# Optimization experiments

Measured on AMD Instinct MI355X. Metric: run time of the kernel, lower is better.

Reference implementation:

```python
import jax, jax.numpy as jnp
import numpy as np

B, S, D, H, F, REF = 4, 1024, 512, 8, 2048, 2
HGRID = 32   # sqrt(seq_len)
HALF = 3     # 7x7 window -> half-width 3


def _masks():
    i = jnp.arange(HGRID)
    near = jnp.abs(i[:, None] - i[None, :]) <= HALF            # [h,h]
    inside = (near[:, None, :, None] & near[None, :, None, :]).reshape(S, S)
    # reverse=True mask (mca): outside-window -> -inf, inside -> 0
    m_rev = jnp.where(inside, 0.0, -jnp.inf).astype(jnp.float32)
    # reverse=False mask (msa/nsa): inside-window -> -inf, outside -> 0 (faithful to source)
    m_fwd = jnp.where(inside, -jnp.inf, 0.0).astype(jnp.float32)
    return m_rev, m_fwd


def _mha(q, k, v, w, b, ow, ob, mask):
    # torch nn.MultiheadAttention, batch_first, eval mode (no dropout)
    hd = D // H
    wq, wk, wv = jnp.split(w, 3, axis=0)
    bq, bk, bv = jnp.split(b, 3)

    def proj(t, wt, bt):
        Bt, Lt = t.shape[0], t.shape[1]
        return (t @ wt.T + bt).reshape(Bt, Lt, H, hd).transpose(0, 2, 1, 3)

    qh, kh, vh = proj(q, wq, bq), proj(k, wk, bk), proj(v, wv, bv)
    scores = jnp.einsum('bhqd,bhkd->bhqk', qh, kh) / jnp.sqrt(jnp.float32(hd))
    if mask is not None:
        scores = scores + mask
    a = jax.nn.softmax(scores, axis=-1)
    o = jnp.einsum('bhqk,bhkd->bhqd', a, vh).transpose(0, 2, 1, 3).reshape(q.shape[0], q.shape[1], D)
    return o @ ow.T + ob


def _ln(x, g, b, eps=1e-5):
    m = x.mean(-1, keepdims=True)
    v = ((x - m) ** 2).mean(-1, keepdims=True)
    return (x - m) / jnp.sqrt(v + eps) * g + b


def setup_inputs() -> dict:
    key = jax.random.key(0)
    ks = jax.random.split(key, 16)
    d = {}
    d['x'] = jax.random.normal(ks[0], (B, S, D), jnp.float32)
    d['ref_mca'] = jax.random.normal(ks[1], (B, REF * S, D), jnp.float32)
    d['gate'] = jax.random.uniform(ks[2], (B, S, 5), jnp.float32)
    i = 3
    for p in ['mca', 'ca', 'msa', 'nsa', 'sa']:
        d[p + '_w'] = 0.02 * jax.random.normal(ks[i], (3 * D, D), jnp.float32); i += 1
        d[p + '_b'] = jnp.zeros((3 * D,), jnp.float32)
        d[p + '_ow'] = 0.02 * jax.random.normal(ks[i], (D, D), jnp.float32); i += 1
        d[p + '_ob'] = jnp.zeros((D,), jnp.float32)
    d['ln1_g'] = jnp.ones((D,), jnp.float32); d['ln1_b'] = jnp.zeros((D,), jnp.float32)
    d['ln2_g'] = jnp.ones((D,), jnp.float32); d['ln2_b'] = jnp.zeros((D,), jnp.float32)
    d['fc1_w'] = 0.02 * jax.random.normal(ks[i], (F, D), jnp.float32); i += 1
    d['fc1_b'] = jnp.zeros((F,), jnp.float32)
    d['fc2_w'] = 0.02 * jax.random.normal(ks[i], (D, F), jnp.float32); i += 1
    d['fc2_b'] = jnp.zeros((D,), jnp.float32)
    return d


def reference(x, ref_mca, gate,
              mca_w, mca_b, mca_ow, mca_ob,
              ca_w, ca_b, ca_ow, ca_ob,
              msa_w, msa_b, msa_ow, msa_ob,
              nsa_w, nsa_b, nsa_ow, nsa_ob,
              sa_w, sa_b, sa_ow, sa_ob,
              ln1_g, ln1_b, ln2_g, ln2_b,
              fc1_w, fc1_b, fc2_w, fc2_b):
    m_rev, m_fwd = _masks()
    # mca branch: sum attention over each seq_len chunk of ref_mca (window-inside mask)
    mca_x = jnp.zeros_like(x)
    for r in range(REF):
        chunk = ref_mca[:, r * S:(r + 1) * S, :]
        mca_x = mca_x + _mha(x, chunk, chunk, mca_w, mca_b, mca_ow, mca_ob, m_rev)
    # faithful to source: loop variable leaks, so ca/nsa use the LAST chunk
    ref_last = ref_mca[:, (REF - 1) * S:, :]
    new_x = gate[:, :, 0:1] * mca_x
    new_x = new_x + gate[:, :, 1:2] * _mha(x, ref_last, ref_last, ca_w, ca_b, ca_ow, ca_ob, None)
    new_x = new_x + gate[:, :, 2:3] * _mha(x, x, x, msa_w, msa_b, msa_ow, msa_ob, m_fwd)
    new_x = new_x + gate[:, :, 3:4] * _mha(x, ref_last, x, nsa_w, nsa_b, nsa_ow, nsa_ob, m_fwd)
    new_x = new_x + gate[:, :, 4:5] * _mha(x, x, x, sa_w, sa_b, sa_ow, sa_ob, None)
    h = _ln(new_x, ln1_g, ln1_b)
    y = jax.nn.gelu(h @ fc1_w.T + fc1_b, approximate=False) @ fc2_w.T + fc2_b
    return _ln(h + y, ln2_g, ln2_b)
```

## Files before the change

### kernel.cpp

```cpp
#include <hip/hip_runtime.h>

typedef __bf16 bf16_t;
typedef bf16_t bf16x8 __attribute__((ext_vector_type(8)));
typedef float f32x4v __attribute__((ext_vector_type(4)));
typedef unsigned int u32;
typedef unsigned long long u64;

__device__ __forceinline__ void gload16(const bf16_t* g, bf16_t* l) {
    __builtin_amdgcn_global_load_lds((const __attribute__((address_space(1))) u32*)g,
                                     (__attribute__((address_space(3))) u32*)l, 16, 0, 0);
}

#define QSCALE 0.18033688011112042f

struct PackBDesc {
    int nseg;
    int blkOf[21];
    const float* src[20];
    bf16_t* dst[20];
    int chunks[20];
    int dstLd[20];
    int shift[20];
};

__global__ __launch_bounds__(256) void packb_k(PackBDesc d) {
    int b = blockIdx.x;
    int s = 0;
    while (s + 1 < d.nseg && b >= d.blkOf[s + 1]) ++s;
    int idx = (b - d.blkOf[s]) * 256 + threadIdx.x;
    if (idx >= d.chunks[s]) return;
    const float* src = d.src[s] + (size_t)idx * 8;
    int r = idx >> d.shift[s];
    int c8 = idx & ((1 << d.shift[s]) - 1);
    bf16_t* dst = d.dst[s] + (size_t)r * d.dstLd[s] + (size_t)c8 * 8;
    float4 v0 = reinterpret_cast<const float4*>(src)[0];
    float4 v1 = reinterpret_cast<const float4*>(src)[1];
    bf16x8 o;
    o[0] = (bf16_t)v0.x; o[1] = (bf16_t)v0.y; o[2] = (bf16_t)v0.z; o[3] = (bf16_t)v0.w;
    o[4] = (bf16_t)v1.x; o[5] = (bf16_t)v1.y; o[6] = (bf16_t)v1.z; o[7] = (bf16_t)v1.w;
    *reinterpret_cast<bf16x8*>(dst) = o;
}

struct PackFDesc {
// ... 109 lines not shown

struct ProjDesc {
    const bf16_t* A[3];
    int aBS[3], aRowOff[3];
    const bf16_t* B[3];
    const float* bias[3];
    bf16_t* Out[3];
    int ldo[3];
    int ntn[3], base[3];
    u64 qmask[3];
};

__global__ __launch_bounds__(256) void proj_k(ProjDesc d) {
    int wg = (blockIdx.x & 7) * 272 + (blockIdx.x >> 3);
    int s = (wg >= d.base[2]) ? 2 : (wg >= d.base[1]) ? 1 : 0;
    int local = wg - d.base[s];
    int tn = local % d.ntn[s];
    int tm = local / d.ntn[s];
    gemm_core<0, 128, 128>(tm, tn, 0, d.A[s], d.aBS[s], d.aRowOff[s], 512,
                           d.B[s], d.bias[s], d.Out[s], d.ldo[s], 0, nullptr, nullptr, 0, 512,
                           d.qmask[s]);
}

template <int EPI, int BM, int BN>
__global__ __launch_bounds__(256) void gemmT(
    const bf16_t* __restrict__ A, int aBS, int aRowOff, int lda,
    const bf16_t* __restrict__ B, const float* __restrict__ bias,
    void* __restrict__ Out, int ldo, size_t outSplitStride,
    const float* __restrict__ gate, const float* __restrict__ obcat, int kPerSplit) {
    gemm_core<EPI, BM, BN>(blockIdx.y, blockIdx.x, blockIdx.z, A, aBS, aRowOff, lda, B, bias,
                           Out, ldo, outSplitStride, gate, obcat, blockIdx.z * kPerSplit, kPerSplit, 0);
}

struct AttnDesc {
    const bf16_t* Q[6];
    const bf16_t* K[6];
    const bf16_t* V[6];
    int ldq[6], ldk[6], ldv[6];
    int segOff[6], gidx[6], mask[6];
    bf16_t* acat;
    const float* gate;
};

__global__ __launch_bounds__(512) void attn7_k(AttnDesc d) {
    __shared__ __attribute__((aligned(16))) bf16_t Ks[2][64][72];
    __shared__ __attribute__((aligned(16))) bf16_t Vt[2][64][72];
    __shared__ __attribute__((aligned(16))) bf16_t Ps[8][16][40];

    const int bid = blockIdx.x;
    const int u = bid % 6;
    const int rem = bid / 6;
    const int qt = rem & 3;
    const int lg = rem >> 2;
    const int h = lg & 7, b = lg >> 3;
    const int mask = d.mask[u];

    const int tid = threadIdx.x;
    const int lane = tid & 63;
    const int w = tid >> 6;
    const int l15 = lane & 15, l16 = lane >> 4;

    const int qbase = qt * 256 + w * 32;
    const int qrow = b * 1024 + qbase;
    const int qblk = qbase >> 5;
    const int ldq = d.ldq[u], ldk = d.ldk[u], ldv = d.ldv[u];

    bf16x8 aq[2][2];
#pragma unroll
    for (int t = 0; t < 2; ++t)
#pragma unroll
        for (int s = 0; s < 2; ++s)
            aq[t][s] = *reinterpret_cast<const bf16x8*>(
                d.Q[u] + (size_t)(qrow + t * 16 + l15) * ldq + h * 64 + s * 32 + l16 * 8);

    float mrow0 = -1e30f, mrow1 = -1e30f, lsum0 = 0.f, lsum1 = 0.f;
    f32x4v accO[2][4] = {};

    const int srow = tid >> 3, scol8 = (tid & 7) * 8;
    const int vcol = srow ^ ((tid & 7) << 3);
    const bf16_t* kbase = d.K[u] + (size_t)(b * 1024) * ldk + h * 64 + scol8;
    const bf16_t* vbase = d.V[u] + (size_t)(b * 1024) * ldv + h * 64 + scol8;

    int t0, t1;
    if (mask == 1) {
        int klo = qt * 8 - 3;  if (klo < 0) klo = 0;
        int khi = qt * 8 + 10; if (khi > 31) khi = 31;
        t0 = klo >> 1; t1 = (khi >> 1) + 1;
    } else { t0 = 0; t1 = 16; }

    auto ldKV = [&](int tt, bf16x8& k, bf16x8& v) {
        k = *reinterpret_cast<const bf16x8*>(kbase + (size_t)(tt * 64 + srow) * ldk);
        v = *reinterpret_cast<const bf16x8*>(vbase + (size_t)(tt * 64 + srow) * ldv);
    };
    auto stKV = [&](int buf, const bf16x8& k, const bf16x8& v) {
        *reinterpret_cast<bf16x8*>(&Ks[buf][srow][scol8]) = k;
#pragma unroll
        for (int j = 0; j < 8; ++j) Vt[buf][scol8 + j][vcol] = v[j];
    };

    bf16x8 rk, rv, rk2, rv2;
    ldKV(t0, rk, rv);
    stKV(0, rk, rv);
    __syncthreads();

    int cur = 0;
    for (int tt = t0; tt < t1; ++tt) {
        if (tt + 1 < t1) ldKV(tt + 1, rk2, rv2);

        int bd0 = qblk - tt * 2;     if (bd0 < 0) bd0 = -bd0;
        int bd1 = qblk - tt * 2 - 1; if (bd1 < 0) bd1 = -bd1;
        const bool a0 = (mask != 1) || (bd0 <= 3);
        const bool a1 = (mask != 1) || (bd1 <= 3);
        if (a0 || a1) {
            f32x4v z[2][4];
#pragma unroll
            for (int nt = 0; nt < 4; ++nt) {
                bf16x8 kf0 = *reinterpret_cast<const bf16x8*>(&Ks[cur][nt * 16 + l15][l16 * 8]);
                bf16x8 kf1 = *reinterpret_cast<const bf16x8*>(&Ks[cur][nt * 16 + l15][32 + l16 * 8]);
                f32x4v z0 = {}, z1 = {};
                z0 = __builtin_amdgcn_mfma_f32_16x16x32_bf16(kf0, aq[0][0], z0, 0, 0, 0);
                z0 = __builtin_amdgcn_mfma_f32_16x16x32_bf16(kf1, aq[0][1], z0, 0, 0, 0);
                z1 = __builtin_amdgcn_mfma_f32_16x16x32_bf16(kf0, aq[1][0], z1, 0, 0, 0);
                z1 = __builtin_amdgcn_mfma_f32_16x16x32_bf16(kf1, aq[1][1], z1, 0, 0, 0);
                z[0][nt] = z0; z[1][nt] = z1;
            }
            float p[2][4][4];
#pragma unroll
            for (int t = 0; t < 2; ++t) {
                const int qgt = t * 16 + l15;
#pragma unroll
                for (int nt = 0; nt < 4; ++nt) {
                    const int bd = (nt >> 1) ? bd1 : bd0;
                    const bool act = (nt >> 1) ? a1 : a0;
                    const bool needMask = (mask == 1) || (mask == 2 && bd <= 3);
#pragma unroll
                    for (int i = 0; i < 4; ++i) {
                        float v = z[t][nt][i];
                        if (!act) v = -1e30f;
                        else if (needMask) {
                            int k5 = (nt & 1) * 16 + l16 * 4 + i;
                            int dq = qgt - k5; if (dq < 0) dq = -dq;
                            bool inside = (bd <= 3) && (dq <= 3);
                            if (mask == 1 ? !inside : inside) v = -1e30f;
                        }
                        p[t][nt][i] = v;
                    }
                }
            }
            float tmx0 = p[0][0][0], tmx1 = p[1][0][0];
#pragma unroll
            for (int nt = 0; nt < 4; ++nt)
#pragma unroll
                for (int i = 0; i < 4; ++i) {
                    tmx0 = fmaxf(tmx0, p[0][nt][i]);
                    tmx1 = fmaxf(tmx1, p[1][nt][i]);
                }
            tmx0 = fmaxf(tmx0, __shfl_xor(tmx0, 16, 64));
            tmx0 = fmaxf(tmx0, __shfl_xor(tmx0, 32, 64));
            tmx1 = fmaxf(tmx1, __shfl_xor(tmx1, 16, 64));
            tmx1 = fmaxf(tmx1, __shfl_xor(tmx1, 32, 64));
            float grow = fmaxf(tmx0 - mrow0, tmx1 - mrow1);
            if (!__all(grow <= 8.0f)) {
                float mn0 = fmaxf(mrow0, tmx0), mn1 = fmaxf(mrow1, tmx1);
                float f0 = exp2f(mrow0 - mn0), f1 = exp2f(mrow1 - mn1);
                mrow0 = mn0; mrow1 = mn1;
                lsum0 *= f0; lsum1 *= f1;
                float fq0[4], fq1[4];
#pragma unroll
                for (int i = 0; i < 4; ++i) {
                    fq0[i] = __shfl(f0, l16 * 4 + i, 64);
                    fq1[i] = __shfl(f1, l16 * 4 + i, 64);
                }
#pragma unroll
                for (int dblk = 0; dblk < 4; ++dblk)
#pragma unroll
                    for (int i = 0; i < 4; ++i) {
                        accO[0][dblk][i] *= fq0[i];
                        accO[1][dblk][i] *= fq1[i];
                    }
            }
            float rs0 = 0.f, rs1 = 0.f;
#pragma unroll
            for (int nt = 0; nt < 4; ++nt)
#pragma unroll
                for (int i = 0; i < 4; ++i) {
                    p[0][nt][i] = exp2f(p[0][nt][i] - mrow0); rs0 += p[0][nt][i];
                    p[1][nt][i] = exp2f(p[1][nt][i] - mrow1); rs1 += p[1][nt][i];
                }
            rs0 += __shfl_xor(rs0, 16, 64); rs0 += __shfl_xor(rs0, 32, 64);
            rs1 += __shfl_xor(rs1, 16, 64); rs1 += __shfl_xor(rs1, 32, 64);
            lsum0 += rs0; lsum1 += rs1;

#pragma unroll
            for (int kh = 0; kh < 2; ++kh) {
#pragma unroll
                for (int n = 0; n < 2; ++n)
#pragma unroll
                    for (int i = 0; i < 4; ++i)
                        Ps[w][l15][n * 16 + l16 * 4 + i] = (bf16_t)p[0][kh * 2 + n][i];
                bf16x8 pa0 = *reinterpret_cast<const bf16x8*>(&Ps[w][l15][l16 * 8]);
#pragma unroll
                for (int n = 0; n < 2; ++n)
#pragma unroll
                    for (int i = 0; i < 4; ++i)
                        Ps[w][l15][n * 16 + l16 * 4 + i] = (bf16_t)p[1][kh * 2 + n][i];
                bf16x8 pa1 = *reinterpret_cast<const bf16x8*>(&Ps[w][l15][l16 * 8]);
#pragma unroll
                for (int dblk = 0; dblk < 4; ++dblk) {
                    int dd = dblk * 16 + l15;
                    int csw = ((kh * 4 + l16) ^ (dd >> 3)) * 8;
                    bf16x8 bv = *reinterpret_cast<const bf16x8*>(&Vt[cur][dd][csw]);
                    accO[0][dblk] = __builtin_amdgcn_mfma_f32_16x16x32_bf16(pa0, bv, accO[0][dblk], 0, 0, 0);
                    accO[1][dblk] = __builtin_amdgcn_mfma_f32_16x16x32_bf16(pa1, bv, accO[1][dblk], 0, 0, 0);
                }
            }
        }

        if (tt + 1 < t1) stKV(cur ^ 1, rk2, rv2);
        __syncthreads();
        cur ^= 1;
    }

    float inv0 = 1.0f / lsum0, inv1 = 1.0f / lsum1;
    float iq0[4], iq1[4];
#pragma unroll
    for (int i = 0; i < 4; ++i) {
        iq0[i] = __shfl(inv0, l16 * 4 + i, 64);
        iq1[i] = __shfl(inv1, l16 * 4 + i, 64);
    }
#pragma unroll
    for (int dblk = 0; dblk < 4; ++dblk)
#pragma unroll
        for (int i = 0; i < 4; ++i) {
            int r0 = qrow + l16 * 4 + i;
            int r1 = r0 + 16;
            float g0 = d.gate[(size_t)r0 * 5 + d.gidx[u]];
            float g1 = d.gate[(size_t)r1 * 5 + d.gidx[u]];
            d.acat[(size_t)r0 * 3072 + d.segOff[u] + h * 64 + dblk * 16 + l15] =
                (bf16_t)(accO[0][dblk][i] * iq0[i] * g0);
            d.acat[(size_t)r1 * 3072 + d.segOff[u] + h * 64 + dblk * 16 + l15] =
                (bf16_t)(accO[1][dblk][i] * iq1[i] * g1);
        }
}

__global__ __launch_bounds__(256) void ln_k(const float* __restrict__ in0,
                                            const float* __restrict__ in1,
                                            const float* __restrict__ in2,
                                            const float* __restrict__ g,
                                            const float* __restrict__ bb,
                                            float* __restrict__ outf,
                                            bf16_t* __restrict__ outb) {
    __shared__ float red[8];
    int row = blockIdx.x;
    int t = threadIdx.x;
    float x0 = in0[(size_t)row * 512 + t];
    float x1 = in0[(size_t)row * 512 + 256 + t];
    if (in1) {
        x0 += in1[(size_t)row * 512 + t];
        x1 += in1[(size_t)row * 512 + 256 + t];
    }
    if (in2) {
        x0 += in2[(size_t)row * 512 + t];
        x1 += in2[(size_t)row * 512 + 256 + t];
    }
    float s = x0 + x1, sq = x0 * x0 + x1 * x1;
#pragma unroll
    for (int d = 1; d < 64; d <<= 1) {
        s += __shfl_xor(s, d, 64);
        sq += __shfl_xor(sq, d, 64);
    }
    int w = t >> 6;
    if ((t & 63) == 0) { red[w] = s; red[4 + w] = sq; }
    __syncthreads();
    s = red[0] + red[1] + red[2] + red[3];
    sq = red[4] + red[5] + red[6] + red[7];
// ... 26 lines not shown
        ow[p] = (const float*)d_in[5 + p * 4];
        ob[p] = (const float*)d_in[6 + p * 4];
    }
    const float* ln1_g = (const float*)d_in[23];
    const float* ln1_b = (const float*)d_in[24];
    const float* ln2_g = (const float*)d_in[25];
    const float* ln2_b = (const float*)d_in[26];
    const float* fc1_w = (const float*)d_in[27];
    const float* fc1_b = (const float*)d_in[28];
    const float* fc2_w = (const float*)d_in[29];
    const float* fc2_b = (const float*)d_in[30];

    char* ws = (char*)d_ws;
    size_t off = 0;
    auto alloc = [&](size_t bytes) {
        char* p = ws + off;
        off += (bytes + 255) & ~(size_t)255;
        return p;
    };
    const size_t S2 = (size_t)4096 * 512;
    bf16_t* xb    = (bf16_t*)alloc(S2 * 2);
    bf16_t* refb  = (bf16_t*)alloc((size_t)8192 * 512 * 2);
    bf16_t* Wxp   = (bf16_t*)alloc((size_t)5120 * 512 * 2);
    bf16_t* WRp   = (bf16_t*)alloc((size_t)2560 * 512 * 2);
    bf16_t* Wop   = (bf16_t*)alloc((size_t)512 * 3072 * 2);
    bf16_t* fc1p  = (bf16_t*)alloc((size_t)2048 * 512 * 2);
    bf16_t* fc2p  = (bf16_t*)alloc((size_t)512 * 2048 * 2);
    float*  bxp   = (float*)alloc((size_t)5120 * 4);
    float*  brp   = (float*)alloc((size_t)2560 * 4);
    float*  obc   = (float*)alloc((size_t)5 * 512 * 4);
    bf16_t* XP    = (bf16_t*)alloc((size_t)4096 * 5120 * 2);
    bf16_t* RP    = (bf16_t*)alloc((size_t)4096 * 2560 * 2);
    bf16_t* R0    = (bf16_t*)alloc((size_t)4096 * 1024 * 2);
    bf16_t* acat  = (bf16_t*)alloc((size_t)4096 * 3072 * 2);
    float*  newx  = (float*)alloc(S2 * 4 * 2);
    float*  hbuf  = (float*)alloc(S2 * 4);
    bf16_t* hb  = refb;
    bf16_t* ub  = XP;
    float*  yp  = newx;

    PackBDesc pb{};
    int nb = 0, blk = 0;
    auto addB = [&](const float* s, bf16_t* dptr, int chunks, int dstLd, int shift) {
        pb.src[nb] = s; pb.dst[nb] = dptr; pb.chunks[nb] = chunks;
        pb.dstLd[nb] = dstLd; pb.shift[nb] = shift;
        pb.blkOf[nb] = blk; blk += (chunks + 255) / 256; ++nb;
    };
    auto addLin = [&](const float* s, bf16_t* dptr, long elems) {
        addB(s, dptr, (int)(elems / 8), 0, 30);
    };
    addLin(x, xb, (long)4096 * 512);
    addLin(ref_mca, refb, (long)8192 * 512);
    addLin(w[0], Wxp, (long)512 * 512);
    addLin(w[1], Wxp + (size_t)512 * 512, (long)512 * 512);
    addLin(w[2], Wxp + (size_t)1024 * 512, (long)1536 * 512);
    addLin(w[3], Wxp + (size_t)2560 * 512, (long)512 * 512);
    addLin(w[3] + (size_t)1024 * 512, Wxp + (size_t)3072 * 512, (long)512 * 512);
    addLin(w[4], Wxp + (size_t)3584 * 512, (long)1536 * 512);
    addLin(w[0] + (size_t)512 * 512, WRp, (long)1024 * 512);
    addLin(w[1] + (size_t)512 * 512, WRp + (size_t)1024 * 512, (long)1024 * 512);
    addLin(w[3] + (size_t)512 * 512, WRp + (size_t)2048 * 512, (long)512 * 512);
    const float* owSeg[6] = {ow[0], ow[0], ow[1], ow[2], ow[3], ow[4]};
    for (int s = 0; s < 6; ++s)
        addB(owSeg[s], Wop + (size_t)s * 512, 32768, 3072, 6);
    addLin(fc1_w, fc1p, (long)2048 * 512);
    addLin(fc2_w, fc2p, (long)512 * 2048);
    pb.nseg = nb; pb.blkOf[nb] = blk;
    packb_k<<<blk, 256, 0, stream>>>(pb);

    PackFDesc pf{};
    int nf = 0, fblk = 0;
    auto addF = [&](const float* s, float* dptr, int n) {
        pf.src[nf] = s; pf.dst[nf] = dptr; pf.n[nf] = n;
        pf.blkOf[nf] = fblk; fblk += (n + 255) / 256; ++nf;
    };
    addF(wb[0], bxp, 512);
    addF(wb[1], bxp + 512, 512);
    addF(wb[2], bxp + 1024, 1536);
    addF(wb[3], bxp + 2560, 512);
    addF(wb[3] + 1024, bxp + 3072, 512);
    addF(wb[4], bxp + 3584, 1536);
    addF(wb[0] + 512, brp, 1024);
    addF(wb[1] + 512, brp + 1024, 1024);
    addF(wb[3] + 512, brp + 2048, 512);
    for (int p = 0; p < 5; ++p) addF(ob[p], obc + p * 512, 512);
    pf.nseg = nf; pf.blkOf[nf] = fblk;
    packf_k<<<fblk, 256, 0, stream>>>(pf);

    ProjDesc pd{};
    pd.A[0] = xb;   pd.aBS[0] = 1024; pd.aRowOff[0] = 0;    pd.B[0] = Wxp; pd.bias[0] = bxp; pd.Out[0] = XP; pd.ldo[0] = 5120; pd.ntn[0] = 40;
    pd.A[1] = refb; pd.aBS[1] = 2048; pd.aRowOff[1] = 1024; pd.B[1] = WRp; pd.bias[1] = brp; pd.Out[1] = RP; pd.ldo[1] = 2560; pd.ntn[1] = 20;
    pd.A[2] = refb; pd.aBS[2] = 2048; pd.aRowOff[2] = 0;    pd.B[2] = WRp; pd.bias[2] = brp; pd.Out[2] = R0; pd.ldo[2] = 1024; pd.ntn[2] = 8;
    pd.base[0] = 0; pd.base[1] = 40 * 32; pd.base[2] = 40 * 32 + 20 * 32;
    pd.qmask[0] = 0xF0F00FFFULL; pd.qmask[1] = 0; pd.qmask[2] = 0;
    proj_k<<<(40 + 20 + 8) * 32, 256, 0, stream>>>(pd);

    AttnDesc ad{};
    auto setU = [&](int u, const bf16_t* Q, int lq, const bf16_t* K, int lk,
                    const bf16_t* V, int lv, int seg, int gi, int mk) {
        ad.Q[u] = Q; ad.ldq[u] = lq; ad.K[u] = K; ad.ldk[u] = lk; ad.V[u] = V; ad.ldv[u] = lv;
        ad.segOff[u] = seg; ad.gidx[u] = gi; ad.mask[u] = mk;
    };
    setU(0, XP, 5120, R0, 1024, R0 + 512, 1024, 0, 0, 1);
    setU(1, XP, 5120, RP, 2560, RP + 512, 2560, 512, 0, 1);
    setU(2, XP + 512, 5120, RP + 1024, 2560, RP + 1536, 2560, 1024, 1, 0);
    setU(3, XP + 1024, 5120, XP + 1536, 5120, XP + 2048, 5120, 1536, 2, 2);
    setU(4, XP + 2560, 5120, RP + 2048, 2560, XP + 3072, 5120, 2048, 3, 2);
    setU(5, XP + 3584, 5120, XP + 4096, 5120, XP + 4608, 5120, 2560, 4, 0);
    ad.acat = acat; ad.gate = gate;
    attn7_k<<<768, 512, 0, stream>>>(ad);

    gemmT<4, 64, 64><<<dim3(8, 64, 2), 256, 0, stream>>>(acat, 1024, 0, 3072, Wop, nullptr,
                                                         newx, 512, S2, gate, obc, 1536);
    ln_k<<<4096, 256, 0, stream>>>(newx, newx + S2, nullptr, ln1_g, ln1_b, hbuf, hb);
    gemmT<1, 128, 128><<<dim3(16, 32, 1), 256, 0, stream>>>(hb, 1024, 0, 512, fc1p, fc1_b,
                                                            ub, 2048, 0, nullptr, nullptr, 512);
    gemmT<3, 64, 64><<<dim3(8, 64, 2), 256, 0, stream>>>(ub, 1024, 0, 2048, fc2p, fc2_b,
                                                         yp, 512, S2, nullptr, nullptr, 1024);
    ln_k<<<4096, 256, 0, stream>>>(hbuf, yp, yp + S2, ln2_g, ln2_b, (float*)d_out, nullptr);
}
```

Before: 351.2 us.

## Pre-transpose V into global buffer and read K/V directly in attention

```diff
diff --git a/kernel.cpp b/kernel.cpp
--- a/kernel.cpp
+++ b/kernel.cpp
@@ -184,26 +184,53 @@
                            Out, ldo, outSplitStride, gate, obcat, blockIdx.z * kPerSplit, kPerSplit, 0);
 }
 
+struct VTDesc {
+    const bf16_t* V[6];
+    int ldv[6];
+    bf16_t* VT;
+};
+
+__global__ __launch_bounds__(256) void vtrans_k(VTDesc d) {
+    __shared__ __attribute__((aligned(16))) bf16_t T[64][72];
+    int bid = blockIdx.x;
+    int kt = bid & 15;
+    int h = (bid >> 4) & 7;
+    int b = (bid >> 7) & 3;
+    int u = bid >> 9;
+    const int ldv = d.ldv[u];
+    const bf16_t* src = d.V[u] + (size_t)(b * 1024 + kt * 64) * ldv + h * 64;
+    int t = threadIdx.x;
+    int r = t >> 2, c0 = (t & 3) * 16;
+    *reinterpret_cast<bf16x8*>(&T[r][c0]) =
+        *reinterpret_cast<const bf16x8*>(src + (size_t)r * ldv + c0);
+    *reinterpret_cast<bf16x8*>(&T[r][c0 + 8]) =
+        *reinterpret_cast<const bf16x8*>(src + (size_t)r * ldv + c0 + 8);
+    __syncthreads();
+    bf16_t* dst = d.VT + (((size_t)u * 4 + b) * 8 + h) * 65536 + (size_t)r * 1024 + kt * 64 + c0;
+    bf16x8 o1, o2;
+#pragma unroll
+    for (int j = 0; j < 8; ++j) { o1[j] = T[c0 + j][r]; o2[j] = T[c0 + 8 + j][r]; }
+    *reinterpret_cast<bf16x8*>(dst) = o1;
+    *reinterpret_cast<bf16x8*>(dst + 8) = o2;
+}
+
 struct AttnDesc {
     const bf16_t* Q[6];
     const bf16_t* K[6];
-    const bf16_t* V[6];
-    int ldq[6], ldk[6], ldv[6];
+    int ldq[6], ldk[6];
     int segOff[6], gidx[6], mask[6];
+    const bf16_t* VT;
     bf16_t* acat;
     const float* gate;
 };
 
-__global__ __launch_bounds__(512) void attn7_k(AttnDesc d) {
-    __shared__ __attribute__((aligned(16))) bf16_t Ks[2][64][72];
-    __shared__ __attribute__((aligned(16))) bf16_t Vt[2][64][72];
-    __shared__ __attribute__((aligned(16))) bf16_t Ps[8][16][40];
+__global__ __launch_bounds__(256) void attn9_k(AttnDesc d) {
+    __shared__ __attribute__((aligned(16))) bf16_t Ps[4][16][40];
 
     const int bid = blockIdx.x;
-    const int u = bid % 6;
-    const int rem = bid / 6;
-    const int qt = rem & 3;
-    const int lg = rem >> 2;
+    const int qt = bid & 7;
+    const int lg = (bid >> 3) & 31;
+    const int u = bid >> 8;
     const int h = lg & 7, b = lg >> 3;
     const int mask = d.mask[u];
 
@@ -212,10 +239,10 @@
     const int w = tid >> 6;
     const int l15 = lane & 15, l16 = lane >> 4;
 
-    const int qbase = qt * 256 + w * 32;
+    const int qbase = qt * 128 + w * 32;
     const int qrow = b * 1024 + qbase;
     const int qblk = qbase >> 5;
-    const int ldq = d.ldq[u], ldk = d.ldk[u], ldv = d.ldv[u];
+    const int ldq = d.ldq[u], ldk = d.ldk[u];
 
     bf16x8 aq[2][2];
 #pragma unroll
@@ -228,149 +255,125 @@
     float mrow0 = -1e30f, mrow1 = -1e30f, lsum0 = 0.f, lsum1 = 0.f;
     f32x4v accO[2][4] = {};
 
-    const int srow = tid >> 3, scol8 = (tid & 7) * 8;
-    const int vcol = srow ^ ((tid & 7) << 3);
-    const bf16_t* kbase = d.K[u] + (size_t)(b * 1024) * ldk + h * 64 + scol8;
-    const bf16_t* vbase = d.V[u] + (size_t)(b * 1024) * ldv + h * 64 + scol8;
+    const bf16_t* kb = d.K[u] + (size_t)(b * 1024) * ldk + h * 64;
+    const bf16_t* vt = d.VT + (((size_t)u * 4 + b) * 8 + h) * 65536;
 
     int t0, t1;
     if (mask == 1) {
-        int klo = qt * 8 - 3;  if (klo < 0) klo = 0;
-        int khi = qt * 8 + 10; if (khi > 31) khi = 31;
+        int klo = qblk - 3; if (klo < 0) klo = 0;
+        int khi = qblk + 3; if (khi > 31) khi = 31;
         t0 = klo >> 1; t1 = (khi >> 1) + 1;
     } else { t0 = 0; t1 = 16; }
 
-    auto ldKV = [&](int tt, bf16x8& k, bf16x8& v) {
-        k = *reinterpret_cast<const bf16x8*>(kbase + (size_t)(tt * 64 + srow) * ldk);
-        v = *reinterpret_cast<const bf16x8*>(vbase + (size_t)(tt * 64 + srow) * ldv);
-    };
-    auto stKV = [&](int buf, const bf16x8& k, const bf16x8& v) {
-        *reinterpret_cast<bf16x8*>(&Ks[buf][srow][scol8]) = k;
-#pragma unroll
-        for (int j = 0; j < 8; ++j) Vt[buf][scol8 + j][vcol] = v[j];
-    };
-
-    bf16x8 rk, rv, rk2, rv2;
-    ldKV(t0, rk, rv);
-    stKV(0, rk, rv);
-    __syncthreads();
-
-    int cur = 0;
     for (int tt = t0; tt < t1; ++tt) {
-        if (tt + 1 < t1) ldKV(tt + 1, rk2, rv2);
-
         int bd0 = qblk - tt * 2;     if (bd0 < 0) bd0 = -bd0;
         int bd1 = qblk - tt * 2 - 1; if (bd1 < 0) bd1 = -bd1;
         const bool a0 = (mask != 1) || (bd0 <= 3);
         const bool a1 = (mask != 1) || (bd1 <= 3);
-        if (a0 || a1) {
-            f32x4v z[2][4];
+        if (!(a0 || a1)) continue;
+
+        f32x4v z[2][4];
+#pragma unroll
+        for (int nt = 0; nt < 4; ++nt) {
+            const bf16_t* kr = kb + (size_t)(tt * 64 + nt * 16 + l15) * ldk + l16 * 8;
+            bf16x8 kf0 = *reinterpret_cast<const bf16x8*>(kr);
+            bf16x8 kf1 = *reinterpret_cast<const bf16x8*>(kr + 32);
+            f32x4v z0 = {}, z1 = {};
+            z0 = __builtin_amdgcn_mfma_f32_16x16x32_bf16(kf0, aq[0][0], z0, 0, 0, 0);
+            z0 = __builtin_amdgcn_mfma_f32_16x16x32_bf16(kf1, aq[0][1], z0, 0, 0, 0);
+            z1 = __builtin_amdgcn_mfma_f32_16x16x32_bf16(kf0, aq[1][0], z1, 0, 0, 0);
+            z1 = __builtin_amdgcn_mfma_f32_16x16x32_bf16(kf1, aq[1][1], z1, 0, 0, 0);
+            z[0][nt] = z0; z[1][nt] = z1;
+        }
+        float p[2][4][4];
+#pragma unroll
+        for (int t = 0; t < 2; ++t) {
+            const int qgt = t * 16 + l15;
 #pragma unroll
             for (int nt = 0; nt < 4; ++nt) {
-                bf16x8 kf0 = *reinterpret_cast<const bf16x8*>(&Ks[cur][nt * 16 + l15][l16 * 8]);
-                bf16x8 kf1 = *reinterpret_cast<const bf16x8*>(&Ks[cur][nt * 16 + l15][32 + l16 * 8]);
-                f32x4v z0 = {}, z1 = {};
-                z0 = __builtin_amdgcn_mfma_f32_16x16x32_bf16(kf0, aq[0][0], z0, 0, 0, 0);
-                z0 = __builtin_amdgcn_mfma_f32_16x16x32_bf16(kf1, aq[0][1], z0, 0, 0, 0);
-                z1 = __builtin_amdgcn_mfma_f32_16x16x32_bf16(kf0, aq[1][0], z1, 0, 0, 0);
-                z1 = __builtin_amdgcn_mfma_f32_16x16x32_bf16(kf1, aq[1][1], z1, 0, 0, 0);
-                z[0][nt] = z0; z[1][nt] = z1;
-            }
-            float p[2][4][4];
-#pragma unroll
-            for (int t = 0; t < 2; ++t) {
-                const int qgt = t * 16 + l15;
-#pragma unroll
-                for (int nt = 0; nt < 4; ++nt) {
-                    const int bd = (nt >> 1) ? bd1 : bd0;
-                    const bool act = (nt >> 1) ? a1 : a0;
-                    const bool needMask = (mask == 1) || (mask == 2 && bd <= 3);
-#pragma unroll
-                    for (int i = 0; i < 4; ++i) {
-                        float v = z[t][nt][i];
-                        if (!act) v = -1e30f;
-                        else if (needMask) {
-                            int k5 = (nt & 1) * 16 + l16 * 4 + i;
-                            int dq = qgt - k5; if (dq < 0) dq = -dq;
-                            bool inside = (bd <= 3) && (dq <= 3);
-                            if (mask == 1 ? !inside : inside) v = -1e30f;
-                        }
-                        p[t][nt][i] = v;
+                const int bd = (nt >> 1) ? bd1 : bd0;
+                const bool act = (nt >> 1) ? a1 : a0;
+                const bool needMask = (mask == 1) || (mask == 2 && bd <= 3);
+#pragma unroll
+                for (int i = 0; i < 4; ++i) {
+                    float v = z[t][nt][i];
+                    if (!act) v = -1e30f;
+                    else if (needMask) {
+                        int k5 = (nt & 1) * 16 + l16 * 4 + i;
+                        int dq = qgt - k5; if (dq < 0) dq = -dq;
+                        bool inside = (bd <= 3) && (dq <= 3);
+                        if (mask == 1 ? !inside : inside) v = -1e30f;
                     }
-                }
-            }
-            float tmx0 = p[0][0][0], tmx1 = p[1][0][0];
-#pragma unroll
-            for (int nt = 0; nt < 4; ++nt)
-#pragma unroll
-                for (int i = 0; i < 4; ++i) {
-                    tmx0 = fmaxf(tmx0, p[0][nt][i]);
-                    tmx1 = fmaxf(tmx1, p[1][nt][i]);
-                }
-            tmx0 = fmaxf(tmx0, __shfl_xor(tmx0, 16, 64));
-            tmx0 = fmaxf(tmx0, __shfl_xor(tmx0, 32, 64));
-            tmx1 = fmaxf(tmx1, __shfl_xor(tmx1, 16, 64));
-            tmx1 = fmaxf(tmx1, __shfl_xor(tmx1, 32, 64));
-            float grow = fmaxf(tmx0 - mrow0, tmx1 - mrow1);
-            if (!__all(grow <= 8.0f)) {
-                float mn0 = fmaxf(mrow0, tmx0), mn1 = fmaxf(mrow1, tmx1);
-                float f0 = exp2f(mrow0 - mn0), f1 = exp2f(mrow1 - mn1);
-                mrow0 = mn0; mrow1 = mn1;
-                lsum0 *= f0; lsum1 *= f1;
-                float fq0[4], fq1[4];
-#pragma unroll
-                for (int i = 0; i < 4; ++i) {
-                    fq0[i] = __shfl(f0, l16 * 4 + i, 64);
-                    fq1[i] = __shfl(f1, l16 * 4 + i, 64);
-                }
-#pragma unroll
-                for (int dblk = 0; dblk < 4; ++dblk)
-#pragma unroll
-                    for (int i = 0; i < 4; ++i) {
-                        accO[0][dblk][i] *= fq0[i];
-                        accO[1][dblk][i] *= fq1[i];
-                    }
-            }
-            float rs0 = 0.f, rs1 = 0.f;
-#pragma unroll
-            for (int nt = 0; nt < 4; ++nt)
-#pragma unroll
-                for (int i = 0; i < 4; ++i) {
-                    p[0][nt][i] = exp2f(p[0][nt][i] - mrow0); rs0 += p[0][nt][i];
-                    p[1][nt][i] = exp2f(p[1][nt][i] - mrow1); rs1 += p[1][nt][i];
-                }
-            rs0 += __shfl_xor(rs0, 16, 64); rs0 += __shfl_xor(rs0, 32, 64);
-            rs1 += __shfl_xor(rs1, 16, 64); rs1 += __shfl_xor(rs1, 32, 64);
-            lsum0 += rs0; lsum1 += rs1;
-
-#pragma unroll
-            for (int kh = 0; kh < 2; ++kh) {
-#pragma unroll
-                for (int n = 0; n < 2; ++n)
-#pragma unroll
-                    for (int i = 0; i < 4; ++i)
-                        Ps[w][l15][n * 16 + l16 * 4 + i] = (bf16_t)p[0][kh * 2 + n][i];
-                bf16x8 pa0 = *reinterpret_cast<const bf16x8*>(&Ps[w][l15][l16 * 8]);
-#pragma unroll
-                for (int n = 0; n < 2; ++n)
-#pragma unroll
-                    for (int i = 0; i < 4; ++i)
-                        Ps[w][l15][n * 16 + l16 * 4 + i] = (bf16_t)p[1][kh * 2 + n][i];
-                bf16x8 pa1 = *reinterpret_cast<const bf16x8*>(&Ps[w][l15][l16 * 8]);
-#pragma unroll
-                for (int dblk = 0; dblk < 4; ++dblk) {
-                    int dd = dblk * 16 + l15;
-                    int csw = ((kh * 4 + l16) ^ (dd >> 3)) * 8;
-                    bf16x8 bv = *reinterpret_cast<const bf16x8*>(&Vt[cur][dd][csw]);
-                    accO[0][dblk] = __builtin_amdgcn_mfma_f32_16x16x32_bf16(pa0, bv, accO[0][dblk], 0, 0, 0);
-                    accO[1][dblk] = __builtin_amdgcn_mfma_f32_16x16x32_bf16(pa1, bv, accO[1][dblk], 0, 0, 0);
+                    p[t][nt][i] = v;
                 }
             }
         }
-
-        if (tt + 1 < t1) stKV(cur ^ 1, rk2, rv2);
-        __syncthreads();
-        cur ^= 1;
+        float tmx0 = p[0][0][0], tmx1 = p[1][0][0];
+#pragma unroll
+        for (int nt = 0; nt < 4; ++nt)
+#pragma unroll
+            for (int i = 0; i < 4; ++i) {
+                tmx0 = fmaxf(tmx0, p[0][nt][i]);
+                tmx1 = fmaxf(tmx1, p[1][nt][i]);
+            }
+        tmx0 = fmaxf(tmx0, __shfl_xor(tmx0, 16, 64));
+        tmx0 = fmaxf(tmx0, __shfl_xor(tmx0, 32, 64));
+        tmx1 = fmaxf(tmx1, __shfl_xor(tmx1, 16, 64));
+        tmx1 = fmaxf(tmx1, __shfl_xor(tmx1, 32, 64));
+        float grow = fmaxf(tmx0 - mrow0, tmx1 - mrow1);
+        if (!__all(grow <= 8.0f)) {
+            float mn0 = fmaxf(mrow0, tmx0), mn1 = fmaxf(mrow1, tmx1);
+            float f0 = exp2f(mrow0 - mn0), f1 = exp2f(mrow1 - mn1);
+            mrow0 = mn0; mrow1 = mn1;
+            lsum0 *= f0; lsum1 *= f1;
+            float fq0[4], fq1[4];
+#pragma unroll
+            for (int i = 0; i < 4; ++i) {
+                fq0[i] = __shfl(f0, l16 * 4 + i, 64);
+                fq1[i] = __shfl(f1, l16 * 4 + i, 64);
+            }
+#pragma unroll
+            for (int dblk = 0; dblk < 4; ++dblk)
+#pragma unroll
+                for (int i = 0; i < 4; ++i) {
+                    accO[0][dblk][i] *= fq0[i];
+                    accO[1][dblk][i] *= fq1[i];
+                }
+        }
+        float rs0 = 0.f, rs1 = 0.f;
+#pragma unroll
+        for (int nt = 0; nt < 4; ++nt)
+#pragma unroll
+            for (int i = 0; i < 4; ++i) {
+                p[0][nt][i] = exp2f(p[0][nt][i] - mrow0); rs0 += p[0][nt][i];
+                p[1][nt][i] = exp2f(p[1][nt][i] - mrow1); rs1 += p[1][nt][i];
+            }
+        rs0 += __shfl_xor(rs0, 16, 64); rs0 += __shfl_xor(rs0, 32, 64);
+        rs1 += __shfl_xor(rs1, 16, 64); rs1 += __shfl_xor(rs1, 32, 64);
+        lsum0 += rs0; lsum1 += rs1;
+
+#pragma unroll
+        for (int kh = 0; kh < 2; ++kh) {
+#pragma unroll
+            for (int n = 0; n < 2; ++n)
+#pragma unroll
+                for (int i = 0; i < 4; ++i)
+                    Ps[w][l15][n * 16 + l16 * 4 + i] = (bf16_t)p[0][kh * 2 + n][i];
+            bf16x8 pa0 = *reinterpret_cast<const bf16x8*>(&Ps[w][l15][l16 * 8]);
+#pragma unroll
+            for (int n = 0; n < 2; ++n)
+#pragma unroll
+                for (int i = 0; i < 4; ++i)
+                    Ps[w][l15][n * 16 + l16 * 4 + i] = (bf16_t)p[1][kh * 2 + n][i];
+            bf16x8 pa1 = *reinterpret_cast<const bf16x8*>(&Ps[w][l15][l16 * 8]);
+#pragma unroll
+            for (int dblk = 0; dblk < 4; ++dblk) {
+                bf16x8 bv = *reinterpret_cast<const bf16x8*>(
+                    vt + (size_t)(dblk * 16 + l15) * 1024 + tt * 64 + kh * 32 + l16 * 8);
+                accO[0][dblk] = __builtin_amdgcn_mfma_f32_16x16x32_bf16(pa0, bv, accO[0][dblk], 0, 0, 0);
+                accO[1][dblk] = __builtin_amdgcn_mfma_f32_16x16x32_bf16(pa1, bv, accO[1][dblk], 0, 0, 0);
+            }
+        }
     }
 
     float inv0 = 1.0f / lsum0, inv1 = 1.0f / lsum1;
@@ -485,6 +488,7 @@
     bf16_t* XP    = (bf16_t*)alloc((size_t)4096 * 5120 * 2);
     bf16_t* RP    = (bf16_t*)alloc((size_t)4096 * 2560 * 2);
     bf16_t* R0    = (bf16_t*)alloc((size_t)4096 * 1024 * 2);
+    bf16_t* VT    = (bf16_t*)alloc((size_t)6 * 4 * 8 * 64 * 1024 * 2);
     bf16_t* acat  = (bf16_t*)alloc((size_t)4096 * 3072 * 2);
     float*  newx  = (float*)alloc(S2 * 4 * 2);
     float*  hbuf  = (float*)alloc(S2 * 4);
@@ -548,20 +552,30 @@
     pd.qmask[0] = 0xF0F00FFFULL; pd.qmask[1] = 0; pd.qmask[2] = 0;
     proj_k<<<(40 + 20 + 8) * 32, 256, 0, stream>>>(pd);
 
+    VTDesc vd{};
+    vd.V[0] = R0 + 512;  vd.ldv[0] = 1024;
+    vd.V[1] = RP + 512;  vd.ldv[1] = 2560;
+    vd.V[2] = RP + 1536; vd.ldv[2] = 2560;
+    vd.V[3] = XP + 2048; vd.ldv[3] = 5120;
+    vd.V[4] = XP + 3072; vd.ldv[4] = 5120;
+    vd.V[5] = XP + 4608; vd.ldv[5] = 5120;
+    vd.VT = VT;
+    vtrans_k<<<3072, 256, 0, stream>>>(vd);
+
     AttnDesc ad{};
     auto setU = [&](int u, const bf16_t* Q, int lq, const bf16_t* K, int lk,
-                    const bf16_t* V, int lv, int seg, int gi, int mk) {
-        ad.Q[u] = Q; ad.ldq[u] = lq; ad.K[u] = K; ad.ldk[u] = lk; ad.V[u] = V; ad.ldv[u] = lv;
+                    int seg, int gi, int mk) {
+        ad.Q[u] = Q; ad.ldq[u] = lq; ad.K[u] = K; ad.ldk[u] = lk;
         ad.segOff[u] = seg; ad.gidx[u] = gi; ad.mask[u] = mk;
     };
-    setU(0, XP, 5120, R0, 1024, R0 + 512, 1024, 0, 0, 1);
-    setU(1, XP, 5120, RP, 2560, RP + 512, 2560, 512, 0, 1);
-    setU(2, XP + 512, 5120, RP + 1024, 2560, RP + 1536, 2560, 1024, 1, 0);
-    setU(3, XP + 1024, 5120, XP + 1536, 5120, XP + 2048, 5120, 1536, 2, 2);
-    setU(4, XP + 2560, 5120, RP + 2048, 2560, XP + 3072, 5120, 2048, 3, 2);
-    setU(5, XP + 3584, 5120, XP + 4096, 5120, XP + 4608, 5120, 2560, 4, 0);
-    ad.acat = acat; ad.gate = gate;
-    attn7_k<<<768, 512, 0, stream>>>(ad);
+    setU(0, XP, 5120, R0, 1024, 0, 0, 1);
+    setU(1, XP, 5120, RP, 2560, 512, 0, 1);
+    setU(2, XP + 512, 5120, RP + 1024, 2560, 1024, 1, 0);
+    setU(3, XP + 1024, 5120, XP + 1536, 5120, 1536, 2, 2);
+    setU(4, XP + 2560, 5120, RP + 2048, 2560, 2048, 3, 2);
+    setU(5, XP + 3584, 5120, XP + 4096, 5120, 2560, 4, 0);
+    ad.VT = VT; ad.acat = acat; ad.gate = gate;
+    attn9_k<<<1536, 256, 0, stream>>>(ad);
 
     gemmT<4, 64, 64><<<dim3(8, 64, 2), 256, 0, stream>>>(acat, 1024, 0, 3072, Wop, nullptr,
                                                          newx, 512, S2, gate, obc, 1536);
```

After: 389.0 us. 10.8% more time.

## Rewrite attention kernel with 32x32 MFMA, register P transpose, async K staging

Applied to the files above, without the earlier changes.

```diff
diff --git a/kernel.cpp b/kernel.cpp
--- a/kernel.cpp
+++ b/kernel.cpp
@@ -3,12 +3,24 @@
 typedef __bf16 bf16_t;
 typedef bf16_t bf16x8 __attribute__((ext_vector_type(8)));
 typedef float f32x4v __attribute__((ext_vector_type(4)));
+typedef float f32x16 __attribute__((ext_vector_type(16)));
 typedef unsigned int u32;
 typedef unsigned long long u64;
 
 __device__ __forceinline__ void gload16(const bf16_t* g, bf16_t* l) {
     __builtin_amdgcn_global_load_lds((const __attribute__((address_space(1))) u32*)g,
                                      (__attribute__((address_space(3))) u32*)l, 16, 0, 0);
+}
+__device__ __forceinline__ u32 pkbf(float a, float b) {
+    union { bf16_t h[2]; u32 u; } v;
+    v.h[0] = (bf16_t)a; v.h[1] = (bf16_t)b;
+    return v.u;
+}
+__device__ __forceinline__ u32 sx32(u32 x) { return (u32)__shfl_xor((int)x, 32, 64); }
+__device__ __forceinline__ bf16x8 mk8(u32 a, u32 b, u32 c, u32 d) {
+    union { u32 u[4]; bf16x8 v; } t;
+    t.u[0] = a; t.u[1] = b; t.u[2] = c; t.u[3] = d;
+    return t.v;
 }
 
 #define QSCALE 0.18033688011112042f
@@ -194,205 +206,193 @@
     const float* gate;
 };
 
-__global__ __launch_bounds__(512) void attn7_k(AttnDesc d) {
-    __shared__ __attribute__((aligned(16))) bf16_t Ks[2][64][72];
-    __shared__ __attribute__((aligned(16))) bf16_t Vt[2][64][72];
-    __shared__ __attribute__((aligned(16))) bf16_t Ps[8][16][40];
+__global__ __launch_bounds__(256) void attn11_k(AttnDesc d) {
+    __shared__ __attribute__((aligned(16))) bf16_t SMEM[16384];
 
     const int bid = blockIdx.x;
-    const int u = bid % 6;
-    const int rem = bid / 6;
-    const int qt = rem & 3;
-    const int lg = rem >> 2;
+    const int qt = bid & 7;
+    const int lg = (bid >> 3) & 31;
+    const int u = bid >> 8;
     const int h = lg & 7, b = lg >> 3;
     const int mask = d.mask[u];
 
     const int tid = threadIdx.x;
     const int lane = tid & 63;
     const int w = tid >> 6;
-    const int l15 = lane & 15, l16 = lane >> 4;
-
-    const int qbase = qt * 256 + w * 32;
+    const int l31 = lane & 31;
+    const int hi = lane >> 5;
+
+    const int qbase = qt * 128 + w * 32;
     const int qrow = b * 1024 + qbase;
     const int qblk = qbase >> 5;
     const int ldq = d.ldq[u], ldk = d.ldk[u], ldv = d.ldv[u];
 
-    bf16x8 aq[2][2];
-#pragma unroll
-    for (int t = 0; t < 2; ++t)
-#pragma unroll
-        for (int s = 0; s < 2; ++s)
-            aq[t][s] = *reinterpret_cast<const bf16x8*>(
-                d.Q[u] + (size_t)(qrow + t * 16 + l15) * ldq + h * 64 + s * 32 + l16 * 8);
-
-    float mrow0 = -1e30f, mrow1 = -1e30f, lsum0 = 0.f, lsum1 = 0.f;
-    f32x4v accO[2][4] = {};
-
-    const int srow = tid >> 3, scol8 = (tid & 7) * 8;
-    const int vcol = srow ^ ((tid & 7) << 3);
-    const bf16_t* kbase = d.K[u] + (size_t)(b * 1024) * ldk + h * 64 + scol8;
-    const bf16_t* vbase = d.V[u] + (size_t)(b * 1024) * ldv + h * 64 + scol8;
+    bf16x8 aq[4];
+#pragma unroll
+    for (int m = 0; m < 4; ++m)
+        aq[m] = *reinterpret_cast<const bf16x8*>(
+            d.Q[u] + (size_t)(qrow + l31) * ldq + h * 64 + m * 16 + hi * 8);
+
+    float mrow = -1e30f, lsum = 0.f;
+    f32x16 acc0 = {}, acc1 = {};
+
+    const bf16_t* kbg = d.K[u] + (size_t)(b * 1024) * ldk + h * 64;
+    const bf16_t* vbg = d.V[u] + (size_t)(b * 1024) * ldv + h * 64;
+
+    const int r1 = w * 8 + (lane >> 3);
+    const int gsw = (lane & 7) ^ (r1 & 7);
+    const int vk = tid >> 2, vdc = (tid & 3) * 16;
 
     int t0, t1;
     if (mask == 1) {
-        int klo = qt * 8 - 3;  if (klo < 0) klo = 0;
-        int khi = qt * 8 + 10; if (khi > 31) khi = 31;
+        int klo = qt * 4 - 3; if (klo < 0) klo = 0;
+        int khi = qt * 4 + 6; if (khi > 31) khi = 31;
         t0 = klo >> 1; t1 = (khi >> 1) + 1;
     } else { t0 = 0; t1 = 16; }
 
-    auto ldKV = [&](int tt, bf16x8& k, bf16x8& v) {
-        k = *reinterpret_cast<const bf16x8*>(kbase + (size_t)(tt * 64 + srow) * ldk);
-        v = *reinterpret_cast<const bf16x8*>(vbase + (size_t)(tt * 64 + srow) * ldv);
-    };
-    auto stKV = [&](int buf, const bf16x8& k, const bf16x8& v) {
-        *reinterpret_cast<bf16x8*>(&Ks[buf][srow][scol8]) = k;
-#pragma unroll
-        for (int j = 0; j < 8; ++j) Vt[buf][scol8 + j][vcol] = v[j];
-    };
-
-    bf16x8 rk, rv, rk2, rv2;
-    ldKV(t0, rk, rv);
-    stKV(0, rk, rv);
+    auto stageK = [&](int buf, int tt) {
+        bf16_t* Ksb = SMEM + buf * 4096;
+        gload16(kbg + (size_t)(tt * 64 + r1) * ldk + gsw * 8, Ksb + w * 512);
+        gload16(kbg + (size_t)(tt * 64 + 32 + r1) * ldk + gsw * 8, Ksb + 2048 + w * 512);
+    };
+    bf16x8 va, vb2;
+    auto loadV = [&](int tt) {
+        const bf16_t* s = vbg + (size_t)(tt * 64 + vk) * ldv + vdc;
+        va = *reinterpret_cast<const bf16x8*>(s);
+        vb2 = *reinterpret_cast<const bf16x8*>(s + 8);
+    };
+    auto writeV = [&](int buf) {
+        bf16_t* Vtb = SMEM + 8192 + buf * 4096;
+#pragma unroll
+        for (int j = 0; j < 8; ++j) {
+            Vtb[(vdc + j) * 64 + (((vk >> 3) ^ j) << 3) + (vk & 7)] = va[j];
+            Vtb[(vdc + 8 + j) * 64 + (((vk >> 3) ^ j) << 3) + (vk & 7)] = vb2[j];
+        }
+    };
+
+    stageK(0, t0);
+    loadV(t0);
+    writeV(0);
     __syncthreads();
 
     int cur = 0;
     for (int tt = t0; tt < t1; ++tt) {
-        if (tt + 1 < t1) ldKV(tt + 1, rk2, rv2);
+        bf16_t* Ksb = SMEM + cur * 4096;
+        bf16_t* Vtb = SMEM + 8192 + cur * 4096;
+        const bool hasNext = (tt + 1 < t1);
+        if (hasNext) { stageK(cur ^ 1, tt + 1); loadV(tt + 1); }
 
         int bd0 = qblk - tt * 2;     if (bd0 < 0) bd0 = -bd0;
         int bd1 = qblk - tt * 2 - 1; if (bd1 < 0) bd1 = -bd1;
         const bool a0 = (mask != 1) || (bd0 <= 3);
         const bool a1 = (mask != 1) || (bd1 <= 3);
         if (a0 || a1) {
-            f32x4v z[2][4];
-#pragma unroll
-            for (int nt = 0; nt < 4; ++nt) {
-                bf16x8 kf0 = *reinterpret_cast<const bf16x8*>(&Ks[cur][nt * 16 + l15][l16 * 8]);
-                bf16x8 kf1 = *reinterpret_cast<const bf16x8*>(&Ks[cur][nt * 16 + l15][32 + l16 * 8]);
-                f32x4v z0 = {}, z1 = {};
-                z0 = __builtin_amdgcn_mfma_f32_16x16x32_bf16(kf0, aq[0][0], z0, 0, 0, 0);
-                z0 = __builtin_amdgcn_mfma_f32_16x16x32_bf16(kf1, aq[0][1], z0, 0, 0, 0);
-                z1 = __builtin_amdgcn_mfma_f32_16x16x32_bf16(kf0, aq[1][0], z1, 0, 0, 0);
-                z1 = __builtin_amdgcn_mfma_f32_16x16x32_bf16(kf1, aq[1][1], z1, 0, 0, 0);
-                z[0][nt] = z0; z[1][nt] = z1;
+            f32x16 c0 = {}, c1 = {};
+#pragma unroll
+            for (int m = 0; m < 4; ++m) {
+                const int g = (((m << 1) + hi) ^ (l31 & 7)) << 3;
+                bf16x8 kf0 = *reinterpret_cast<const bf16x8*>(Ksb + l31 * 64 + g);
+                bf16x8 kf1 = *reinterpret_cast<const bf16x8*>(Ksb + (32 + l31) * 64 + g);
+                c0 = __builtin_amdgcn_mfma_f32_32x32x16_bf16(kf0, aq[m], c0, 0, 0, 0);
+                c1 = __builtin_amdgcn_mfma_f32_32x32x16_bf16(kf1, aq[m], c1, 0, 0, 0);
             }
-            float p[2][4][4];
-#pragma unroll
-            for (int t = 0; t < 2; ++t) {
-                const int qgt = t * 16 + l15;
-#pragma unroll
-                for (int nt = 0; nt < 4; ++nt) {
-                    const int bd = (nt >> 1) ? bd1 : bd0;
-                    const bool act = (nt >> 1) ? a1 : a0;
-                    const bool needMask = (mask == 1) || (mask == 2 && bd <= 3);
-#pragma unroll
-                    for (int i = 0; i < 4; ++i) {
-                        float v = z[t][nt][i];
-                        if (!act) v = -1e30f;
-                        else if (needMask) {
-                            int k5 = (nt & 1) * 16 + l16 * 4 + i;
-                            int dq = qgt - k5; if (dq < 0) dq = -dq;
-                            bool inside = (bd <= 3) && (dq <= 3);
-                            if (mask == 1 ? !inside : inside) v = -1e30f;
-                        }
-                        p[t][nt][i] = v;
+#pragma unroll
+            for (int kb2 = 0; kb2 < 2; ++kb2) {
+                const int bd = kb2 ? bd1 : bd0;
+                const bool act = kb2 ? a1 : a0;
+                const bool nm = (mask == 1) || (mask == 2 && bd <= 3);
+#pragma unroll
+                for (int r = 0; r < 16; ++r) {
+                    float v = kb2 ? c1[r] : c0[r];
+                    if (!act) v = -1e30f;
+                    else if (nm) {
+                        int krow = (r & 3) + 8 * (r >> 2) + 4 * hi;
+                        int dq = l31 - krow; if (dq < 0) dq = -dq;
+                        bool inside = (bd <= 3) && (dq <= 3);
+                        if (mask == 1 ? !inside : inside) v = -1e30f;
+                    }
+                    if (kb2) c1[r] = v; else c0[r] = v;
+                }
+            }
+            float tmx = c0[0];
+#pragma unroll
+            for (int r = 1; r < 16; ++r) tmx = fmaxf(tmx, c0[r]);
+#pragma unroll
+            for (int r = 0; r < 16; ++r) tmx = fmaxf(tmx, c1[r]);
+            tmx = fmaxf(tmx, __shfl_xor(tmx, 32, 64));
+            if (!__all(tmx - mrow <= 8.0f)) {
+                float mn = fmaxf(mrow, tmx);
+                float fac = exp2f(mrow - mn);
+                mrow = mn; lsum *= fac;
+#pragma unroll
+                for (int r = 0; r < 16; ++r) { acc0[r] *= fac; acc1[r] *= fac; }
+            }
+            float rs = 0.f;
+#pragma unroll
+            for (int r = 0; r < 16; ++r) { c0[r] = exp2f(c0[r] - mrow); rs += c0[r]; }
+#pragma unroll
+            for (int r = 0; r < 16; ++r) { c1[r] = exp2f(c1[r] - mrow); rs += c1[r]; }
+            rs += __shfl_xor(rs, 32, 64);
+            lsum += rs;
+
+#pragma unroll
+            for (int kb2 = 0; kb2 < 2; ++kb2) {
+                u32 P0, P1, P2, P3, P4, P5, P6, P7;
+                if (kb2 == 0) {
+                    P0 = pkbf(c0[0], c0[1]);   P1 = pkbf(c0[2], c0[3]);
+                    P2 = pkbf(c0[4], c0[5]);   P3 = pkbf(c0[6], c0[7]);
+                    P4 = pkbf(c0[8], c0[9]);   P5 = pkbf(c0[10], c0[11]);
+                    P6 = pkbf(c0[12], c0[13]); P7 = pkbf(c0[14], c0[15]);
+                } else {
+                    P0 = pkbf(c1[0], c1[1]);   P1 = pkbf(c1[2], c1[3]);
+                    P2 = pkbf(c1[4], c1[5]);   P3 = pkbf(c1[6], c1[7]);
+                    P4 = pkbf(c1[8], c1[9]);   P5 = pkbf(c1[10], c1[11]);
+                    P6 = pkbf(c1[12], c1[13]); P7 = pkbf(c1[14], c1[15]);
+                }
+                u32 X0 = sx32(P0), X1 = sx32(P1), X2 = sx32(P2), X3 = sx32(P3);
+                u32 X4 = sx32(P4), X5 = sx32(P5), X6 = sx32(P6), X7 = sx32(P7);
+                bf16x8 pb0 = hi ? mk8(X2, X3, P2, P3) : mk8(P0, P1, X0, X1);
+                bf16x8 pb1 = hi ? mk8(X6, X7, P6, P7) : mk8(P4, P5, X4, X5);
+                const int st0 = kb2 * 2, st1 = st0 + 1;
+#pragma unroll
+                for (int db = 0; db < 2; ++db) {
+                    const int vrow = (db * 32 + l31) * 64;
+                    const int sw = (l31 & 7);
+                    bf16x8 vf0 = *reinterpret_cast<const bf16x8*>(
+                        Vtb + vrow + ((((st0 << 1) + hi) ^ sw) << 3));
+                    bf16x8 vf1 = *reinterpret_cast<const bf16x8*>(
+                        Vtb + vrow + ((((st1 << 1) + hi) ^ sw) << 3));
+                    if (db == 0) {
+                        acc0 = __builtin_amdgcn_mfma_f32_32x32x16_bf16(vf0, pb0, acc0, 0, 0, 0);
+                        acc0 = __builtin_amdgcn_mfma_f32_32x32x16_bf16(vf1, pb1, acc0, 0, 0, 0);
+                    } else {
+                        acc1 = __builtin_amdgcn_mfma_f32_32x32x16_bf16(vf0, pb0, acc1, 0, 0, 0);
+                        acc1 = __builtin_amdgcn_mfma_f32_32x32x16_bf16(vf1, pb1, acc1, 0, 0, 0);
                     }
                 }
             }
-            float tmx0 = p[0][0][0], tmx1 = p[1][0][0];
-#pragma unroll
-            for (int nt = 0; nt < 4; ++nt)
-#pragma unroll
-                for (int i = 0; i < 4; ++i) {
-                    tmx0 = fmaxf(tmx0, p[0][nt][i]);
-                    tmx1 = fmaxf(tmx1, p[1][nt][i]);
-                }
-            tmx0 = fmaxf(tmx0, __shfl_xor(tmx0, 16, 64));
-            tmx0 = fmaxf(tmx0, __shfl_xor(tmx0, 32, 64));
-            tmx1 = fmaxf(tmx1, __shfl_xor(tmx1, 16, 64));
-            tmx1 = fmaxf(tmx1, __shfl_xor(tmx1, 32, 64));
-            float grow = fmaxf(tmx0 - mrow0, tmx1 - mrow1);
-            if (!__all(grow <= 8.0f)) {
-                float mn0 = fmaxf(mrow0, tmx0), mn1 = fmaxf(mrow1, tmx1);
-                float f0 = exp2f(mrow0 - mn0), f1 = exp2f(mrow1 - mn1);
-                mrow0 = mn0; mrow1 = mn1;
-                lsum0 *= f0; lsum1 *= f1;
-                float fq0[4], fq1[4];
-#pragma unroll
-                for (int i = 0; i < 4; ++i) {
-                    fq0[i] = __shfl(f0, l16 * 4 + i, 64);
-                    fq1[i] = __shfl(f1, l16 * 4 + i, 64);
-                }
-#pragma unroll
-                for (int dblk = 0; dblk < 4; ++dblk)
-#pragma unroll
-                    for (int i = 0; i < 4; ++i) {
-                        accO[0][dblk][i] *= fq0[i];
-                        accO[1][dblk][i] *= fq1[i];
-                    }
-            }
-            float rs0 = 0.f, rs1 = 0.f;
-#pragma unroll
-            for (int nt = 0; nt < 4; ++nt)
-#pragma unroll
-                for (int i = 0; i < 4; ++i) {
-                    p[0][nt][i] = exp2f(p[0][nt][i] - mrow0); rs0 += p[0][nt][i];
-                    p[1][nt][i] = exp2f(p[1][nt][i] - mrow1); rs1 += p[1][nt][i];
-                }
-            rs0 += __shfl_xor(rs0, 16, 64); rs0 += __shfl_xor(rs0, 32, 64);
-            rs1 += __shfl_xor(rs1, 16, 64); rs1 += __shfl_xor(rs1, 32, 64);
-            lsum0 += rs0; lsum1 += rs1;
-
-#pragma unroll
-            for (int kh = 0; kh < 2; ++kh) {
-#pragma unroll
-                for (int n = 0; n < 2; ++n)
-#pragma unroll
-                    for (int i = 0; i < 4; ++i)
-                        Ps[w][l15][n * 16 + l16 * 4 + i] = (bf16_t)p[0][kh * 2 + n][i];
-                bf16x8 pa0 = *reinterpret_cast<const bf16x8*>(&Ps[w][l15][l16 * 8]);
-#pragma unroll
-                for (int n = 0; n < 2; ++n)
-#pragma unroll
-                    for (int i = 0; i < 4; ++i)
-                        Ps[w][l15][n * 16 + l16 * 4 + i] = (bf16_t)p[1][kh * 2 + n][i];
-                bf16x8 pa1 = *reinterpret_cast<const bf16x8*>(&Ps[w][l15][l16 * 8]);
-#pragma unroll
-                for (int dblk = 0; dblk < 4; ++dblk) {
-                    int dd = dblk * 16 + l15;
-                    int csw = ((kh * 4 + l16) ^ (dd >> 3)) * 8;
-                    bf16x8 bv = *reinterpret_cast<const bf16x8*>(&Vt[cur][dd][csw]);
-                    accO[0][dblk] = __builtin_amdgcn_mfma_f32_16x16x32_bf16(pa0, bv, accO[0][dblk], 0, 0, 0);
-                    accO[1][dblk] = __builtin_amdgcn_mfma_f32_16x16x32_bf16(pa1, bv, accO[1][dblk], 0, 0, 0);
-                }
-            }
         }
-
-        if (tt + 1 < t1) stKV(cur ^ 1, rk2, rv2);
+        if (hasNext) writeV(cur ^ 1);
         __syncthreads();
         cur ^= 1;
     }
 
-    float inv0 = 1.0f / lsum0, inv1 = 1.0f / lsum1;
-    float iq0[4], iq1[4];
-#pragma unroll
-    for (int i = 0; i < 4; ++i) {
-        iq0[i] = __shfl(inv0, l16 * 4 + i, 64);
-        iq1[i] = __shfl(inv1, l16 * 4 + i, 64);
-    }
-#pragma unroll
-    for (int dblk = 0; dblk < 4; ++dblk)
-#pragma unroll
-        for (int i = 0; i < 4; ++i) {
-            int r0 = qrow + l16 * 4 + i;
-            int r1 = r0 + 16;
-            float g0 = d.gate[(size_t)r0 * 5 + d.gidx[u]];
-            float g1 = d.gate[(size_t)r1 * 5 + d.gidx[u]];
-            d.acat[(size_t)r0 * 3072 + d.segOff[u] + h * 64 + dblk * 16 + l15] =
-                (bf16_t)(accO[0][dblk][i] * iq0[i] * g0);
-            d.acat[(size_t)r1 * 3072 + d.segOff[u] + h * 64 + dblk * 16 + l15] =
-                (bf16_t)(accO[1][dblk][i] * iq1[i] * g1);
-        }
+    float sc = (1.0f / lsum) * d.gate[(size_t)(qrow + l31) * 5 + d.gidx[u]];
+    bf16_t* OS = SMEM;
+    const int qloc = w * 32 + l31;
+#pragma unroll
+    for (int r = 0; r < 16; ++r) {
+        int drow = (r & 3) + 8 * (r >> 2) + 4 * hi;
+        OS[qloc * 72 + drow] = (bf16_t)(acc0[r] * sc);
+        OS[qloc * 72 + 32 + drow] = (bf16_t)(acc1[r] * sc);
+    }
+    __syncthreads();
+    const int orow = tid >> 1, ocb = (tid & 1) * 32;
+    bf16_t* dst = d.acat + (size_t)(b * 1024 + qt * 128 + orow) * 3072 + d.segOff[u] + h * 64 + ocb;
+#pragma unroll
+    for (int i = 0; i < 4; ++i)
+        *reinterpret_cast<bf16x8*>(dst + i * 8) =
+            *reinterpret_cast<const bf16x8*>(OS + orow * 72 + ocb + i * 8);
 }
 
 __global__ __launch_bounds__(256) void ln_k(const float* __restrict__ in0,
@@ -561,7 +561,7 @@
     setU(4, XP + 2560, 5120, RP + 2048, 2560, XP + 3072, 5120, 2048, 3, 2);
     setU(5, XP + 3584, 5120, XP + 4096, 5120, XP + 4608, 5120, 2560, 4, 0);
     ad.acat = acat; ad.gate = gate;
-    attn7_k<<<768, 512, 0, stream>>>(ad);
+    attn11_k<<<1536, 256, 0, stream>>>(ad);
 
     gemmT<4, 64, 64><<<dim3(8, 64, 2), 256, 0, stream>>>(acat, 1024, 0, 3072, Wop, nullptr,
                                                          newx, 512, S2, gate, obc, 1536);
```

Result: faster. 333.8 us (-4.9%).
